# Optimization experiments

Measured on AMD Instinct MI355X. Metric: run time of the kernel, lower is better.

## Reference

```python
import jax, jax.numpy as jnp
import numpy as np

SHAPE = 64
K = 8
HID = 512
OUT = K + 2 * K * SHAPE + 2 * SHAPE  # 1160
B, T = 32, 2048


def setup_inputs() -> dict:
    key = jax.random.key(0)
    ks = jax.random.split(key, 4)
    x = jax.random.normal(ks[0], (B, T, SHAPE), dtype=jnp.float32)
    W1 = jax.random.normal(ks[1], (SHAPE, HID), dtype=jnp.float32) / np.sqrt(SHAPE)
    b1 = jnp.zeros((HID,), dtype=jnp.float32)
    W2 = jax.random.normal(ks[2], (HID, HID), dtype=jnp.float32) / np.sqrt(HID)
    b2 = jnp.zeros((HID,), dtype=jnp.float32)
    W3 = jax.random.normal(ks[3], (HID, OUT), dtype=jnp.float32) / np.sqrt(HID) * 0.1
    b3 = jnp.zeros((OUT,), dtype=jnp.float32)
    return {"x": x, "W1": W1, "b1": b1, "W2": W2, "b2": b2, "W3": W3, "b3": b3}


def _coupling_forward(x, W1, b1, W2, b2, W3, b3):
    # coupling mask over feature dim: first half conditions the second half
    mask = jnp.zeros((SHAPE,), dtype=x.dtype).at[:SHAPE // 2].set(1.0)  # [D]
    x_ = x * mask  # [B,T,D]

    # conditioner MLP
    h = jax.nn.relu(x_ @ W1 + b1)
    h = jax.nn.relu(h @ W2 + b2)
    params = h @ W3 + b3  # [B,T,OUT]

    logscales = params[..., :SHAPE]
    biases = params[..., SHAPE:2 * SHAPE]
    mdn = params[..., 2 * SHAPE:]
    logits = mdn[..., :K]                                   # [B,T,K]
    mu = mdn[..., K:K + K * SHAPE].reshape(*x.shape[:2], K, SHAPE)
    logstd = mdn[..., K + K * SHAPE:].reshape(*x.shape[:2], K, SHAPE)

    # --- MixtureCDFFlow.flow ---
    weights = jax.nn.softmax(logits, axis=-1)[..., None]    # [B,T,K,1]
    std = jnp.exp(logstd)
    u = (x[:, :, None, :] - mu) / std                       # [B,T,K,D]
    cdf = 0.5 * (1.0 + jax.lax.erf(u / np.sqrt(2.0)))
    z = jnp.sum(cdf * weights, axis=2)                      # [B,T,D]
    pdf = jnp.exp(-0.5 * u * u) / (std * np.sqrt(2.0 * np.pi))
    logd_mix = jnp.log(jnp.sum(pdf * weights, axis=2))      # [B,T,D]

    # --- Inverse(Sigmoid).flow == Sigmoid.invert ---
    xs = -jnp.log(1.0 / z - 1.0)
    logd_sig = -jnp.log(z) - jnp.log(1.0 - z)

    # --- ElemwiseAffine.flow ---
    out = xs * jnp.exp(logscales) + biases
    log_det = logd_mix + logd_sig + logscales

    x_out = (1.0 - mask) * out + x_
    log_det = log_det * (1.0 - mask)
    return x_out, log_det


def reference(x, W1, b1, W2, b2, W3, b3):
    return _coupling_forward(x, W1, b1, W2, b2, W3, b3)
```

## Files before the change

### kernel.cpp

```cpp
#include <hip/hip_runtime.h>

typedef short short8 __attribute__((ext_vector_type(8)));
typedef float f32x4 __attribute__((ext_vector_type(4)));

#define NROWS 65536
#define NCOMPACT 640

__device__ __forceinline__ short f2bf(float f) {
  union { float f; unsigned u; } c; c.f = f;
  unsigned r = (c.u + 0x7fffu + ((c.u >> 16) & 1u)) >> 16;
  return (short)r;
}

__device__ __forceinline__ float fastrcp(float a) {
  float r; asm("v_rcp_f32 %0, %1" : "=v"(r) : "v"(a)); return r;
}

__device__ __forceinline__ int w3col(int n) {
  if (n < 32)  return 32 + n;
  if (n < 64)  return 96 + (n - 32);
  if (n < 72)  return 128 + (n - 64);
  if (n < 96)  return -1;
  if (n < 352) { int q = n - 96;  return 168 + (q >> 5) * 64 + (q & 31); }
  if (n < 608) { int q = n - 352; return 680 + (q >> 5) * 64 + (q & 31); }
  return -1;
}

__global__ __launch_bounds__(256) void prep_w_kernel(
    const float* __restrict__ W1, const float* __restrict__ W2,
    const float* __restrict__ W3, const float* __restrict__ b3,
    short* __restrict__ w1t, short* __restrict__ w2t,
    short* __restrict__ w3t, float* __restrict__ b3c) {
  const int NW1 = 512 * 32, NW2 = 512 * 512, NW3 = NCOMPACT * 512;
  int t = blockIdx.x * 256 + threadIdx.x;
  if (t < NW1) {
    int n = t >> 5, k = t & 31;
    w1t[t] = f2bf(W1[k * 512 + n]);
  } else if (t < NW1 + NW2) {
    int i = t - NW1; int n = i >> 9, k = i & 511;
    w2t[i] = f2bf(W2[k * 512 + n]);
  } else if (t < NW1 + NW2 + NW3) {
    int i = t - NW1 - NW2; int n = i >> 9, k = i & 511;
    int c = w3col(n);
    w3t[i] = (c >= 0) ? f2bf(W3[(size_t)k * 1160 + c]) : (short)0;
  } else if (t < NW1 + NW2 + NW3 + NCOMPACT) {
    int n = t - NW1 - NW2 - NW3;
    int c = w3col(n);
    b3c[n] = (c >= 0) ? b3[c] : 0.0f;
  }
}

#define SSTR 40
__global__ __launch_bounds__(256, 4) void g12_kernel(
    const float* __restrict__ x,
    const short* __restrict__ w1t,
    const float* __restrict__ b1,
    const short* __restrict__ w2t,
    const float* __restrict__ b2,
    short* __restrict__ h2) {
  __shared__ __attribute__((aligned(16))) short Bs[2][128 * 32];
  __shared__ __attribute__((aligned(16))) short W1b[2][32 * 32];
  __shared__ __attribute__((aligned(16))) short Sx[4][32 * SSTR];
  const int tid = threadIdx.x;
  const int cpx = gridDim.x >> 3;
  const int s = blockIdx.x;
  const int w = (s & 7) * cpx + (s >> 3);
  const int m0 = (w >> 2) * 128, n0 = (w & 3) * 128;
  const int lane = tid & 63, wid = tid >> 6;
  const int lr = lane & 15, hi = lane >> 4, lk = hi * 8;

  short8 xcf[2];
#pragma unroll
  for (int mi = 0; mi < 2; ++mi) {
    int row = m0 + wid * 32 + mi * 16 + lr;
    const float* xs = x + (size_t)row * 64 + lk;
    f32x4 v0 = *(const f32x4*)xs;
    f32x4 v1 = *(const f32x4*)(xs + 4);
    short8 v;
#pragma unroll
    for (int i = 0; i < 4; ++i) { v[i] = f2bf(v0[i]); v[4 + i] = f2bf(v1[i]); }
    xcf[mi] = v;
  }

  auto STAGE_B = [&](int buf, int kt) {
#pragma unroll
    for (int base = wid * 64; base < 512; base += 256) {
      int c = base + lane;
      int row = c >> 2;
      int skb = ((c & 3) ^ ((row >> 1) & 3)) << 4;
      const char* g = (const char*)(w2t + (size_t)(n0 + row) * 512 + kt) + skb;
      __builtin_amdgcn_global_load_lds(
          (const __attribute__((address_space(1))) void*)g,
          (__attribute__((address_space(3))) void*)((char*)Bs[buf] + base * 16),
          16, 0, 0);
    }
  };
  auto STAGE_W1 = [&](int buf, int kt) {
    if (wid < 2) {
      int c = wid * 64 + lane;
      int row = c >> 2;
      int skb = ((c & 3) ^ ((row >> 1) & 3)) << 4;
      const char* g = (const char*)(w1t + (size_t)(kt + row) * 32) + skb;
      __builtin_amdgcn_global_load_lds(
          (const __attribute__((address_space(1))) void*)g,
          (__attribute__((address_space(3))) void*)((char*)W1b[buf] + wid * 1024),
          16, 0, 0);
    }
  };

  short8 af[2];
  auto H1STEP = [&](int buf, int kt) {
    const short* Wb = W1b[buf];
    short8 wf[2];
#pragma unroll
    for (int ni = 0; ni < 2; ++ni) {
      int row = ni * 16 + lr;
      wf[ni] = *(const short8*)(&Wb[row * 32 + (lk ^ (((row >> 1) & 3) << 3))]);
    }
    f32x4 a1[2][2] = {};
#pragma unroll
    for (int mi = 0; mi < 2; ++mi)
#pragma unroll
      for (int ni = 0; ni < 2; ++ni)
        a1[mi][ni] = __builtin_amdgcn_mfma_f32_16x16x32_bf16(
            xcf[mi], wf[ni], a1[mi][ni], 0, 0, 0);
    short* S = Sx[wid];
#pragma unroll
    for (int ni = 0; ni < 2; ++ni) {
      int acol = ni * 16 + lr;
      float bv = b1[kt + acol];
#pragma unroll
      for (int mi = 0; mi < 2; ++mi)
#pragma unroll
        for (int j = 0; j < 4; ++j)
          S[(mi * 16 + hi * 4 + j) * SSTR + acol] =
              f2bf(fmaxf(a1[mi][ni][j] + bv, 0.0f));
    }
#pragma unroll
    for (int mi = 0; mi < 2; ++mi)
      af[mi] = *(const short8*)(&S[(mi * 16 + lr) * SSTR + lk]);
  };

  f32x4 acc[2][8] = {};
  auto COMPUTE = [&](int buf) {
#pragma unroll
    for (int ni = 0; ni < 8; ++ni) {
      int row = ni * 16 + lr;
      short8 bf_ = *(const short8*)(&Bs[buf][row * 32 + (lk ^ (((row >> 1) & 3) << 3))]);
      acc[0][ni] = __builtin_amdgcn_mfma_f32_16x16x32_bf16(af[0], bf_, acc[0][ni], 0, 0, 0);
      acc[1][ni] = __builtin_amdgcn_mfma_f32_16x16x32_bf16(af[1], bf_, acc[1][ni], 0, 0, 0);
    }
  };

  STAGE_B(0, 0); STAGE_W1(0, 0);
  __syncthreads();
  for (int t = 0; t < 16; ++t) {
    int pb = t & 1;
    if (t < 15) { STAGE_B(pb ^ 1, (t + 1) * 32); STAGE_W1(pb ^ 1, (t + 1) * 32); }
    H1STEP(pb, t * 32);
    COMPUTE(pb);
    __syncthreads();
  }

#pragma unroll
  for (int ni = 0; ni < 8; ++ni) {
    int col = n0 + ni * 16 + lr;
    float bv = b2[col];
#pragma unroll
    for (int mi = 0; mi < 2; ++mi) {
#pragma unroll
      for (int j = 0; j < 4; ++j) {
        int row = m0 + wid * 32 + mi * 16 + hi * 4 + j;
        h2[(size_t)row * 512 + col] = f2bf(fmaxf(acc[mi][ni][j] + bv, 0.0f));
      }
    }
  }
}

#define PSTR 644
#define BUF1 49152
__global__ __launch_bounds__(1024, 4) void gemm3_fused_kernel(
    const short* __restrict__ A,
    const short* __restrict__ Bw,
    const float* __restrict__ b3c,
    const float* __restrict__ x,
    float* __restrict__ out) {
  __shared__ __attribute__((aligned(16))) char lds[98304];
  const int tid = threadIdx.x;
  const int m0 = blockIdx.x * 128;
  const int lane = tid & 63, wid = tid >> 6;
  const int wr = wid >> 2, wc = wid & 3;
  const int lr = lane & 15, hi = lane >> 4, lk = hi * 8;

  f32x4 acc[2][10] = {};

  auto STAGE = [&](int bo, int kt) {
#pragma unroll
    for (int base = wid * 64; base < 3072; base += 1024) {
      int c = base + lane;
      char* dst = lds + bo + (size_t)base * 16;
      if (base < 512) {
        int row = c >> 2;
        int skb = ((c & 3) ^ ((row >> 1) & 3)) << 4;
        const char* ga = (const char*)(A + (size_t)(m0 + row) * 512 + kt) + skb;
        __builtin_amdgcn_global_load_lds(
            (const __attribute__((address_space(1))) void*)ga,
            (__attribute__((address_space(3))) void*)dst, 16, 0, 0);
      } else {
        int q = c - 512;
        int row = q >> 2;
        int skb = ((q & 3) ^ ((row >> 1) & 3)) << 4;
        const char* gb = (const char*)(Bw + (size_t)row * 512 + kt) + skb;
        __builtin_amdgcn_global_load_lds(
            (const __attribute__((address_space(1))) void*)gb,
            (__attribute__((address_space(3))) void*)dst, 16, 0, 0);
      }
    }
  };

  auto COMPUTE = [&](int bo) {
    const short* As = (const short*)(lds + bo);
    const short* Bs = (const short*)(lds + bo + 8192);
    short8 af[2];
#pragma unroll
    for (int mi = 0; mi < 2; ++mi) {
      int row = wr * 32 + mi * 16 + lr;
      int k = lk ^ (((row >> 1) & 3) << 3);
      af[mi] = *(const short8*)(&As[row * 32 + k]);
    }
#pragma unroll
    for (int ni = 0; ni < 10; ++ni) {
      int brow = wc * 160 + ni * 16 + lr;
      int k = lk ^ (((brow >> 1) & 3) << 3);
      short8 bf_ = *(const short8*)(&Bs[brow * 32 + k]);
      acc[0][ni] = __builtin_amdgcn_mfma_f32_16x16x32_bf16(af[0], bf_, acc[0][ni], 0, 0, 0);
      acc[1][ni] = __builtin_amdgcn_mfma_f32_16x16x32_bf16(af[1], bf_, acc[1][ni], 0, 0, 0);
    }
  };

  STAGE(0, 0);
  __syncthreads();
  for (int t = 0; t < 16; t += 2) {
    STAGE(BUF1, (t + 1) * 32);
    COMPUTE(0);
    __syncthreads();
    if (t < 14) STAGE(0, (t + 2) * 32);
    COMPUTE(BUF1);
    __syncthreads();
  }

  float* plds = (float*)lds;
  float* xo  = out;
  float* ldo = out + (size_t)NROWS * 64;
#pragma unroll
  for (int p = 0; p < 4; ++p) {
    if (p) __syncthreads();
    if (wr == p) {
#pragma unroll
      for (int mi = 0; mi < 2; ++mi) {
#pragma unroll
        for (int ni = 0; ni < 10; ++ni) {
          int col = wc * 160 + ni * 16 + lr;
          float bv = b3c[col];
#pragma unroll
          for (int j = 0; j < 4; ++j)
            plds[(mi * 16 + hi * 4 + j) * PSTR + col] = acc[mi][ni][j] + bv;
        }
      }
    }
    __syncthreads();
    {
      int rl = tid >> 5, j = tid & 31;
      const float* p_ = plds + rl * PSTR;
      int grow = m0 + p * 32 + rl;

      float lg[8];
#pragma unroll
      for (int k = 0; k < 8; ++k) lg[k] = p_[64 + k];
      float mx = lg[0];
#pragma unroll
      for (int k = 1; k < 8; ++k) mx = fmaxf(mx, lg[k]);
      float wgt[8], wsum = 0.0f;
#pragma unroll
      for (int k = 0; k < 8; ++k) { wgt[k] = __expf(lg[k] - mx); wsum += wgt[k]; }

      float xd = x[(size_t)grow * 64 + 32 + j];
      float zs = 0.0f, ps = 0.0f;
#pragma unroll
      for (int k = 0; k < 8; ++k) {
        float mu   = p_[96 + k * 32 + j];
        float lstd = p_[352 + k * 32 + j];
        float istd = __expf(-lstd);
        float u = (xd - mu) * istd;
        float x2 = 0.5f * u * u;
        float e  = __expf(-x2);
        ps += wgt[k] * e * istd;
        float ax = fabsf(u) * 0.70710678118654752f;
        float t_ = fastrcp(fmaf(0.5f, ax, 1.0f));
        float poly = -1.26551223f + t_*(1.00002368f + t_*(0.37409196f +
                     t_*(0.09678418f + t_*(-0.18628806f + t_*(0.27886807f +
                     t_*(-1.13520398f + t_*(1.48851587f + t_*(-0.82215223f +
                     t_*0.17087277f))))))));
        float erfc_half = 0.5f * t_ * __expf(poly - x2);
        float cdf = (u >= 0.0f) ? 1.0f - erfc_half : erfc_half;
        zs += wgt[k] * cdf;
      }
      float winv = fastrcp(wsum);
      float z  = zs * winv;
      float pm = ps * winv * 0.39894228040143268f;
      float logz = __logf(z), log1mz = __logf(1.0f - z);
      float ls = p_[j], bv = p_[32 + j];
      float outv = (logz - log1mz) * __expf(ls) + bv;
      float ld = __logf(pm) - logz - log1mz + ls;

      size_t base = (size_t)grow * 64;
      xo[base + j]       = x[base + j];
      xo[base + 32 + j]  = outv;
      ldo[base + j]      = 0.0f;
      ldo[base + 32 + j] = ld;
    }
  }
}

extern "C" void kernel_launch(void* const* d_in, const int* in_sizes, int n_in,
                              void* d_out, int out_size, void* d_ws, size_t ws_size,
                              hipStream_t stream) {
  const float* x  = (const float*)d_in[0];
  const float* W1 = (const float*)d_in[1];
  const float* b1 = (const float*)d_in[2];
  const float* W2 = (const float*)d_in[3];
  const float* b2 = (const float*)d_in[4];
  const float* W3 = (const float*)d_in[5];
  const float* b3 = (const float*)d_in[6];
  char* ws = (char*)d_ws;

  short* h2  = (short*)ws;
  short* w1t = (short*)(ws + 67108864);
  short* w2t = (short*)(ws + 67141632);
  short* w3t = (short*)(ws + 67665920);
  float* b3c = (float*)(ws + 68321280);
  float* out = (float*)d_out;

  {
    int total = 512 * 32 + 512 * 512 + NCOMPACT * 512 + NCOMPACT;
    prep_w_kernel<<<(total + 255) / 256, 256, 0, stream>>>(W1, W2, W3, b3, w1t, w2t, w3t, b3c);
  }
  g12_kernel<<<2048, 256, 0, stream>>>(x, w1t, b1, w2t, b2, h2);
  gemm3_fused_kernel<<<NROWS / 128, 1024, 0, stream>>>(h2, w3t, b3c, x, out);
}
```

Measured before the change: 133.6 us.

## Split fused GEMM3 epilogue kernel into two N-halves per row tile

The compacted W3 columns are reordered so each half of the 640-wide output holds everything needed for 16 of the 32 transformed features. Logits are duplicated into both halves. The fused GEMM3 plus mixture-CDF kernel now launches two 512-thread blocks per 128-row tile, each computing one 320-column half. This cuts LDS per block from 96KB to 56KB and doubles the block count, aiming for more resident blocks per CU and better latency hiding. In exchange, the A (h2) tile is loaded twice and the softmax over the logits is computed redundantly in each half.

```diff
diff --git a/kernel.cpp b/kernel.cpp
--- a/kernel.cpp
+++ b/kernel.cpp
@@ -16,13 +16,14 @@
   float r; asm("v_rcp_f32 %0, %1" : "=v"(r) : "v"(a)); return r;
 }
 
-__device__ __forceinline__ int w3col(int n) {
-  if (n < 32)  return 32 + n;
-  if (n < 64)  return 96 + (n - 32);
-  if (n < 72)  return 128 + (n - 64);
-  if (n < 96)  return -1;
-  if (n < 352) { int q = n - 96;  return 168 + (q >> 5) * 64 + (q & 31); }
-  if (n < 608) { int q = n - 352; return 680 + (q >> 5) * 64 + (q & 31); }
+__device__ __forceinline__ int w3col2(int n) {
+  int h = n / 320, m = n % 320;
+  if (m < 16)  return 32 + 16 * h + m;
+  if (m < 32)  return 96 + 16 * h + (m - 16);
+  if (m < 40)  return 128 + (m - 32);
+  if (m < 48)  return -1;
+  if (m < 176) { int q = m - 48;  return 168 + (q >> 4) * 64 + 16 * h + (q & 15); }
+  if (m < 304) { int q = m - 176; return 680 + (q >> 4) * 64 + 16 * h + (q & 15); }
   return -1;
 }
 
@@ -41,11 +42,11 @@
     w2t[i] = f2bf(W2[k * 512 + n]);
   } else if (t < NW1 + NW2 + NW3) {
     int i = t - NW1 - NW2; int n = i >> 9, k = i & 511;
-    int c = w3col(n);
+    int c = w3col2(n);
     w3t[i] = (c >= 0) ? f2bf(W3[(size_t)k * 1160 + c]) : (short)0;
   } else if (t < NW1 + NW2 + NW3 + NCOMPACT) {
     int n = t - NW1 - NW2 - NW3;
-    int c = w3col(n);
+    int c = w3col2(n);
     b3c[n] = (c >= 0) ? b3[c] : 0.0f;
   }
 }
@@ -177,26 +178,26 @@
   }
 }
 
-#define PSTR 644
-#define BUF1 49152
-__global__ __launch_bounds__(1024, 4) void gemm3_fused_kernel(
+#define PSTR2 324
+#define HBUF 28672
+__global__ __launch_bounds__(512, 4) void gemm3_fused_kernel(
     const short* __restrict__ A,
     const short* __restrict__ Bw,
     const float* __restrict__ b3c,
     const float* __restrict__ x,
     float* __restrict__ out) {
-  __shared__ __attribute__((aligned(16))) char lds[98304];
+  __shared__ __attribute__((aligned(16))) char lds[57344];
   const int tid = threadIdx.x;
-  const int m0 = blockIdx.x * 128;
+  const int m0 = (blockIdx.x >> 1) * 128;
+  const int half = blockIdx.x & 1, bn0 = half * 320;
   const int lane = tid & 63, wid = tid >> 6;
-  const int wr = wid >> 2, wc = wid & 3;
+  const int wr = wid >> 1, wc = wid & 1;
   const int lr = lane & 15, hi = lane >> 4, lk = hi * 8;
 
   f32x4 acc[2][10] = {};
 
   auto STAGE = [&](int bo, int kt) {
-#pragma unroll
-    for (int base = wid * 64; base < 3072; base += 1024) {
+    for (int base = wid * 64; base < 1792; base += 512) {
       int c = base + lane;
       char* dst = lds + bo + (size_t)base * 16;
       if (base < 512) {
@@ -210,7 +211,7 @@
         int q = c - 512;
         int row = q >> 2;
         int skb = ((q & 3) ^ ((row >> 1) & 3)) << 4;
-        const char* gb = (const char*)(Bw + (size_t)row * 512 + kt) + skb;
+        const char* gb = (const char*)(Bw + (size_t)(bn0 + row) * 512 + kt) + skb;
         __builtin_amdgcn_global_load_lds(
             (const __attribute__((address_space(1))) void*)gb,
             (__attribute__((address_space(3))) void*)dst, 16, 0, 0);
@@ -241,11 +242,11 @@
   STAGE(0, 0);
   __syncthreads();
   for (int t = 0; t < 16; t += 2) {
-    STAGE(BUF1, (t + 1) * 32);
+    STAGE(HBUF, (t + 1) * 32);
     COMPUTE(0);
     __syncthreads();
     if (t < 14) STAGE(0, (t + 2) * 32);
-    COMPUTE(BUF1);
+    COMPUTE(HBUF);
     __syncthreads();
   }
 
@@ -261,22 +262,23 @@
 #pragma unroll
         for (int ni = 0; ni < 10; ++ni) {
           int col = wc * 160 + ni * 16 + lr;
-          float bv = b3c[col];
+          float bv = b3c[bn0 + col];
 #pragma unroll
           for (int j = 0; j < 4; ++j)
-            plds[(mi * 16 + hi * 4 + j) * PSTR + col] = acc[mi][ni][j] + bv;
+            plds[(mi * 16 + hi * 4 + j) * PSTR2 + col] = acc[mi][ni][j] + bv;
         }
       }
     }
     __syncthreads();
     {
-      int rl = tid >> 5, j = tid & 31;
-      const float* p_ = plds + rl * PSTR;
+      int rl = tid >> 4, jj = tid & 15;
+      int j = half * 16 + jj;
+      const float* p_ = plds + rl * PSTR2;
       int grow = m0 + p * 32 + rl;
 
       float lg[8];
 #pragma unroll
-      for (int k = 0; k < 8; ++k) lg[k] = p_[64 + k];
+      for (int k = 0; k < 8; ++k) lg[k] = p_[32 + k];
       float mx = lg[0];
 #pragma unroll
       for (int k = 1; k < 8; ++k) mx = fmaxf(mx, lg[k]);
@@ -288,8 +290,8 @@
       float zs = 0.0f, ps = 0.0f;
 #pragma unroll
       for (int k = 0; k < 8; ++k) {
-        float mu   = p_[96 + k * 32 + j];
-        float lstd = p_[352 + k * 32 + j];
+        float mu   = p_[48 + k * 16 + jj];
+        float lstd = p_[176 + k * 16 + jj];
         float istd = __expf(-lstd);
         float u = (xd - mu) * istd;
         float x2 = 0.5f * u * u;
@@ -309,8 +311,8 @@
       float z  = zs * winv;
       float pm = ps * winv * 0.39894228040143268f;
       float logz = __logf(z), log1mz = __logf(1.0f - z);
-      float ls = p_[j], bv = p_[32 + j];
-      float outv = (logz - log1mz) * __expf(ls) + bv;
+      float ls = p_[jj], bvb = p_[16 + jj];
+      float outv = (logz - log1mz) * __expf(ls) + bvb;
       float ld = __logf(pm) - logz - log1mz + ls;
 
       size_t base = (size_t)grow * 64;
@@ -346,5 +348,5 @@
     prep_w_kernel<<<(total + 255) / 256, 256, 0, stream>>>(W1, W2, W3, b3, w1t, w2t, w3t, b3c);
   }
   g12_kernel<<<2048, 256, 0, stream>>>(x, w1t, b1, w2t, b2, h2);
-  gemm3_fused_kernel<<<NROWS / 128, 1024, 0, stream>>>(h2, w3t, b3c, x, out);
-}
+  gemm3_fused_kernel<<<(NROWS / 128) * 2, 512, 0, stream>>>(h2, w3t, b3c, x, out);
+}
```

Measured after the change: 139.2 us. +4.2%, slower.
